# Kernel optimization log

Hardware: AMD Instinct MI355X
Metric: run time of the kernel (lower is better)

Reference implementation:

```python
import jax, jax.numpy as jnp
import numpy as np

N, D, H, T = 262144, 128, 256, 4  # nodes, embed_dim, hidden_dim, num node types


def setup_inputs() -> dict:
    key = jax.random.key(0)
    ks = jax.random.split(key, 5)
    h = jax.random.normal(ks[0], (N, D), dtype=jnp.float32)
    message = jax.random.normal(ks[1], (N, D), dtype=jnp.float32)
    node_type_ids = jax.random.randint(ks[2], (N,), 0, T, dtype=jnp.int32)
    # Spectrally-normalized linear weights are just fixed matrices at eval time;
    # scale so spectral norm is O(1).
    W1 = jax.random.normal(ks[3], (T, 2 * D, H), dtype=jnp.float32) / np.sqrt(2 * D)
    b1 = jnp.zeros((T, H), dtype=jnp.float32)
    W2 = jax.random.normal(ks[4], (T, H, D), dtype=jnp.float32) / np.sqrt(H)
    b2 = jnp.zeros((T, D), dtype=jnp.float32)
    return {"h": h, "message": message, "node_type_ids": node_type_ids,
            "W1": W1, "b1": b1, "W2": W2, "b2": b2}


def reference(h, message, node_type_ids, W1, b1, W2, b2):
    # x : (N, 2d) concatenated node state and message
    x = jnp.concatenate([h, message], axis=-1)
    dh = jnp.zeros_like(h)
    # Loop over the small fixed set of node types (T=4); each iteration is a
    # dense 2-layer SiLU MLP, results routed back by boolean mask (the torch
    # code's gather -> MLP -> scatter, expressed as compute-all + select).
    for t in range(T):
        y = jax.nn.silu(x @ W1[t] + b1[t]) @ W2[t] + b2[t]  # (N, d)
        mask = (node_type_ids == t)[:, None]
        dh = jnp.where(mask, y, dh)
    return dh
```

## Files before the change

### kernel.cpp

```cpp
#include <hip/hip_runtime.h>
#include <hip/hip_bf16.h>
#include <stdint.h>

#define N_NODES 262144
#define DDIM 128
#define KDIM 256
#define HDIM 256
#define NTYPE 4
#define BM 64
#define NB 1024

typedef float  f32x4  __attribute__((ext_vector_type(4)));
typedef short  bf16x8 __attribute__((ext_vector_type(8)));
typedef unsigned short u16x4 __attribute__((ext_vector_type(4)));


__device__ __forceinline__ unsigned short f2b(float v) {
    unsigned int u = __builtin_bit_cast(unsigned int, v);
    u += 0x7FFFu + ((u >> 16) & 1u);
    return (unsigned short)(u >> 16);
}

__global__ void k_prep(const float* __restrict__ W1, const float* __restrict__ W2,
                       unsigned short* __restrict__ W1T, unsigned short* __restrict__ W2T) {
    int tid = blockIdx.x * blockDim.x + threadIdx.x;
    const int n1 = NTYPE * HDIM * KDIM;
    for (int i = tid; i < n1; i += gridDim.x * blockDim.x) {
        int t = i / (HDIM * KDIM);
        int rem = i % (HDIM * KDIM);
        int hh = rem / KDIM;
        int k  = rem % KDIM;
        W1T[i] = f2b(W1[((size_t)t * KDIM + k) * HDIM + hh]);
    }
    const int n2 = NTYPE * DDIM * HDIM;
    for (int i = tid; i < n2; i += gridDim.x * blockDim.x) {
        int t = i / (DDIM * HDIM);
        int rem = i % (DDIM * HDIM);
        int d = rem / HDIM;
        int k = rem % HDIM;
        W2T[i] = f2b(W2[((size_t)t * HDIM + k) * DDIM + d]);
    }
}

__global__ void k_hist(const int* __restrict__ ids, int* __restrict__ bcnt) {
    __shared__ int cnt[NTYPE];
    int tid = threadIdx.x, lane = tid & 63;
    if (tid < NTYPE) cnt[tid] = 0;
    __syncthreads();
    int t = ids[blockIdx.x * 256 + tid];
    #pragma unroll
    for (int tt = 0; tt < NTYPE; ++tt) {
        unsigned long long m = __ballot(t == tt);
        if (lane == 0) atomicAdd(&cnt[tt], (int)__popcll(m));
    }
    __syncthreads();
    if (tid < NTYPE) bcnt[tid * NB + blockIdx.x] = cnt[tid];
}

__global__ __launch_bounds__(1024) void k_scan(const int* __restrict__ bcnt,
                                               int* __restrict__ gbase, int* __restrict__ meta) {
    __shared__ int wpart[16];
    __shared__ int ttot[NTYPE + 1];
    int tid = threadIdx.x, lane = tid & 63, wv = tid >> 6;
    if (tid == 0) ttot[0] = 0;
    for (int t = 0; t < NTYPE; ++t) {
        int v = bcnt[t * NB + tid];
        int s = v;
        #pragma unroll
        for (int d = 1; d < 64; d <<= 1) {
            int u = __shfl_up(s, d, 64);
            if (lane >= d) s += u;
        }
        if (lane == 63) wpart[wv] = s;
        __syncthreads();
        if (tid == 0) {
            int a = 0;
            for (int w = 0; w < 16; ++w) { int x = wpart[w]; wpart[w] = a; a += x; }
            ttot[t + 1] = ttot[t] + a;
        }
        __syncthreads();
        gbase[t * NB + tid] = ttot[t] + wpart[wv] + (s - v);
        __syncthreads();
    }
    if (tid == 0) {
        int off = 0, toff = 0;
        for (int t = 0; t < NTYPE; ++t) {
            int c = ttot[t + 1] - ttot[t];
            meta[4 + t] = off;
            meta[9 + t] = toff;
            off  += c;
            toff += (c + BM - 1) / BM;
        }
        meta[8]  = off;
        meta[13] = toff;
    }
}

__global__ void k_scatter(const int* __restrict__ ids, const int* __restrict__ gbase,
                          int* __restrict__ perm) {
    __shared__ int wb[4][NTYPE];
    int tid = threadIdx.x, lane = tid & 63, wv = tid >> 6;
    int i = blockIdx.x * 256 + tid;
    int t = ids[i];
    #pragma unroll
    for (int tt = 0; tt < NTYPE; ++tt) {
        unsigned long long m = __ballot(t == tt);
        if (lane == 0) wb[wv][tt] = (int)__popcll(m);
    }
    __syncthreads();
    if (tid < NTYPE) {
        int a = 0;
        for (int w = 0; w < 4; ++w) { int x = wb[w][tid]; wb[w][tid] = a; a += x; }
    }
    __syncthreads();
    #pragma unroll
    for (int tt = 0; tt < NTYPE; ++tt) {
        unsigned long long m = __ballot(t == tt);
        if (t == tt) {
            int rank = (int)__popcll(m & ((1ull << lane) - 1ull));
            perm[gbase[tt * NB + blockIdx.x] + wb[wv][tt] + rank] = i;
        }
    }
}

__global__ __launch_bounds__(256) void k_mlp(
        const float* __restrict__ hbuf, const float* __restrict__ mbuf,
        const float* __restrict__ b1,   const float* __restrict__ b2,
        const int* __restrict__ meta,   const int* __restrict__ perm,
        const unsigned short* __restrict__ W1T, const unsigned short* __restrict__ W2T,
        float* __restrict__ dh) {
    __shared__ unsigned short lds[BM * KDIM];

    int b = blockIdx.x;
    if (b >= meta[13]) return;
    int t = 0;
    #pragma unroll
    for (int tt = 1; tt < NTYPE; ++tt) t += (b >= meta[9 + tt]);
    int row0   = meta[4 + t] + (b - meta[9 + t]) * BM;
    int segend = meta[4 + t + 1];

    int tid = threadIdx.x, lane = tid & 63, w = tid >> 6;
    int lr = lane & 15, lg = lane >> 4;

    int c = lane;
    #pragma unroll
    for (int j = 0; j < 16; ++j) {
        int r = w + 4 * j;
        int p = row0 + r;
        int node = perm[p < N_NODES ? p : N_NODES - 1];
        const float* src = (c < 32) ? (hbuf + (size_t)node * DDIM + c * 4)
                                    : (mbuf + (size_t)node * DDIM + (c - 32) * 4);
        float4 v = *reinterpret_cast<const float4*>(src);
        u16x4 o;
        o.x = f2b(v.x); o.y = f2b(v.y); o.z = f2b(v.z); o.w = f2b(v.w);
        int soff = (r * KDIM + c * 4) ^ ((r & 7) << 3);
        *reinterpret_cast<u16x4*>(&lds[soff]) = o;
    }
    __syncthreads();

    f32x4 acc[4][4];
    #pragma unroll
    for (int ht = 0; ht < 4; ++ht)
        #pragma unroll
        for (int mt = 0; mt < 4; ++mt)
            acc[ht][mt] = (f32x4){0.f, 0.f, 0.f, 0.f};

    const unsigned short* W1p = W1T + (size_t)t * HDIM * KDIM + (size_t)(w * 64) * KDIM;
    #pragma unroll
    for (int kt = 0; kt < KDIM / 32; ++kt) {
        int kk = kt * 32 + lg * 8;
        bf16x8 aw[4], xb[4];
        #pragma unroll
        for (int ht = 0; ht < 4; ++ht)
            aw[ht] = *reinterpret_cast<const bf16x8*>(W1p + (size_t)(ht * 16 + lr) * KDIM + kk);
        #pragma unroll
        for (int mt = 0; mt < 4; ++mt) {
            int r = mt * 16 + lr;
            int soff = (r * KDIM + kk) ^ ((r & 7) << 3);
            xb[mt] = *reinterpret_cast<const bf16x8*>(&lds[soff]);
        }
        #pragma unroll
        for (int ht = 0; ht < 4; ++ht)
            #pragma unroll
            for (int mt = 0; mt < 4; ++mt)
                acc[ht][mt] = __builtin_amdgcn_mfma_f32_16x16x32_bf16(aw[ht], xb[mt], acc[ht][mt], 0, 0, 0);
    }
    __syncthreads();

    #pragma unroll
    for (int ht = 0; ht < 4; ++ht) {
        int hcol = w * 64 + ht * 16 + lg * 4;
        f32x4 b1v = *reinterpret_cast<const f32x4*>(&b1[t * HDIM + hcol]);
        #pragma unroll
        for (int mt = 0; mt < 4; ++mt) {
            int m = mt * 16 + lr;
            u16x4 o;
            #pragma unroll
            for (int r4 = 0; r4 < 4; ++r4) {
                float z = acc[ht][mt][r4] + b1v[r4];
                float s = z / (1.f + __expf(-z));
                o[r4] = f2b(s);
            }
            int soff = (m * KDIM + hcol) ^ ((m & 7) << 3);
            *reinterpret_cast<u16x4*>(&lds[soff]) = o;
        }
    }
    __syncthreads();

    f32x4 acc2[2][4];
    #pragma unroll
    for (int dt = 0; dt < 2; ++dt)
        #pragma unroll
        for (int mt = 0; mt < 4; ++mt)
            acc2[dt][mt] = (f32x4){0.f, 0.f, 0.f, 0.f};

    const unsigned short* W2p = W2T + (size_t)t * DDIM * HDIM + (size_t)(w * 32) * HDIM;
    #pragma unroll
    for (int kt = 0; kt < HDIM / 32; ++kt) {
        int kk = kt * 32 + lg * 8;
        bf16x8 aw[2], ab[4];
        #pragma unroll
        for (int dt = 0; dt < 2; ++dt)
            aw[dt] = *reinterpret_cast<const bf16x8*>(W2p + (size_t)(dt * 16 + lr) * HDIM + kk);
        #pragma unroll
        for (int mt = 0; mt < 4; ++mt) {
            int m = mt * 16 + lr;
            int soff = (m * KDIM + kk) ^ ((m & 7) << 3);
            ab[mt] = *reinterpret_cast<const bf16x8*>(&lds[soff]);
        }
        #pragma unroll
        for (int dt = 0; dt < 2; ++dt)
            #pragma unroll
            for (int mt = 0; mt < 4; ++mt)
                acc2[dt][mt] = __builtin_amdgcn_mfma_f32_16x16x32_bf16(aw[dt], ab[mt], acc2[dt][mt], 0, 0, 0);
    }

    int nd[4];
    #pragma unroll
    for (int mt = 0; mt < 4; ++mt) {
        int p = row0 + mt * 16 + lr;
        nd[mt] = perm[p < N_NODES ? p : N_NODES - 1];
    }
    #pragma unroll
    for (int dt = 0; dt < 2; ++dt) {
        int d0 = w * 32 + dt * 16 + lg * 4;
        f32x4 b2v = *reinterpret_cast<const f32x4*>(&b2[t * DDIM + d0]);
        #pragma unroll
        for (int mt = 0; mt < 4; ++mt) {
            int p = row0 + mt * 16 + lr;
            if (p < segend) {
                f32x4 v = acc2[dt][mt] + b2v;
                *reinterpret_cast<f32x4*>(&dh[(size_t)nd[mt] * DDIM + d0]) = v;
            }
        }
    }
}

extern "C" void kernel_launch(void* const* d_in, const int* in_sizes, int n_in,
                              void* d_out, int out_size, void* d_ws, size_t ws_size,
                              hipStream_t stream) {
    const float* h   = (const float*)d_in[0];
    const float* msg = (const float*)d_in[1];
    const int*   ids = (const int*)d_in[2];
    const float* W1  = (const float*)d_in[3];
    const float* b1  = (const float*)d_in[4];
    const float* W2  = (const float*)d_in[5];
    const float* b2  = (const float*)d_in[6];
    float* dh = (float*)d_out;

    char* ws = (char*)d_ws;
    int* meta  = (int*)ws;
    int* perm  = (int*)(ws + 128);
    int* bcnt  = (int*)(ws + 128 + (size_t)N_NODES * 4);
    int* gbase = bcnt + NTYPE * NB;
    unsigned short* W1T = (unsigned short*)(gbase + NTYPE * NB);
    unsigned short* W2T = W1T + (size_t)NTYPE * HDIM * KDIM;

    k_prep<<<512, 256, 0, stream>>>(W1, W2, W1T, W2T);
    k_hist<<<NB, 256, 0, stream>>>(ids, bcnt);
    k_scan<<<1, 1024, 0, stream>>>(bcnt, gbase, meta);
    k_scatter<<<NB, 256, 0, stream>>>(ids, gbase, perm);
    k_mlp<<<N_NODES / BM + NTYPE, 256, 0, stream>>>(h, msg, b1, b2, meta, perm, W1T, W2T, dh);
}
```

Baseline: 451.9 us.

## Fuse prep and histogram kernels, split LDS buffers, batch weight loads in MLP

Merges the weight-transpose kernel and the type histogram into one launch, with extra blocks handling the weight conversion, which saves one launch. In the MLP kernel, the activation tile gets its own LDS buffer instead of reusing the input tile buffer, so one barrier can be dropped. W1 fragments are now loaded in batches of four k-steps and all W2 fragments are preloaded before the second GEMM, aiming to overlap global loads with compute. This raises register and LDS use (64 KB per block), and launch_bounds(256,2) asks for two blocks per CU, which may force register spills.

```diff
diff --git a/kernel.cpp b/kernel.cpp
--- a/kernel.cpp
+++ b/kernel.cpp
@@ -21,40 +21,43 @@
     return (unsigned short)(u >> 16);
 }
 
-__global__ void k_prep(const float* __restrict__ W1, const float* __restrict__ W2,
-                       unsigned short* __restrict__ W1T, unsigned short* __restrict__ W2T) {
-    int tid = blockIdx.x * blockDim.x + threadIdx.x;
-    const int n1 = NTYPE * HDIM * KDIM;
-    for (int i = tid; i < n1; i += gridDim.x * blockDim.x) {
-        int t = i / (HDIM * KDIM);
-        int rem = i % (HDIM * KDIM);
-        int hh = rem / KDIM;
-        int k  = rem % KDIM;
-        W1T[i] = f2b(W1[((size_t)t * KDIM + k) * HDIM + hh]);
-    }
-    const int n2 = NTYPE * DDIM * HDIM;
-    for (int i = tid; i < n2; i += gridDim.x * blockDim.x) {
-        int t = i / (DDIM * HDIM);
-        int rem = i % (DDIM * HDIM);
-        int d = rem / HDIM;
-        int k = rem % HDIM;
-        W2T[i] = f2b(W2[((size_t)t * HDIM + k) * DDIM + d]);
-    }
-}
-
-__global__ void k_hist(const int* __restrict__ ids, int* __restrict__ bcnt) {
+__global__ void k_prep_hist(const int* __restrict__ ids,
+                            const float* __restrict__ W1, const float* __restrict__ W2,
+                            int* __restrict__ bcnt,
+                            unsigned short* __restrict__ W1T, unsigned short* __restrict__ W2T) {
     __shared__ int cnt[NTYPE];
-    int tid = threadIdx.x, lane = tid & 63;
-    if (tid < NTYPE) cnt[tid] = 0;
-    __syncthreads();
-    int t = ids[blockIdx.x * 256 + tid];
-    #pragma unroll
-    for (int tt = 0; tt < NTYPE; ++tt) {
-        unsigned long long m = __ballot(t == tt);
-        if (lane == 0) atomicAdd(&cnt[tt], (int)__popcll(m));
-    }
-    __syncthreads();
-    if (tid < NTYPE) bcnt[tid * NB + blockIdx.x] = cnt[tid];
+    if (blockIdx.x < NB) {
+        int tid = threadIdx.x, lane = tid & 63;
+        if (tid < NTYPE) cnt[tid] = 0;
+        __syncthreads();
+        int t = ids[blockIdx.x * 256 + tid];
+        #pragma unroll
+        for (int tt = 0; tt < NTYPE; ++tt) {
+            unsigned long long m = __ballot(t == tt);
+            if (lane == 0) atomicAdd(&cnt[tt], (int)__popcll(m));
+        }
+        __syncthreads();
+        if (tid < NTYPE) bcnt[tid * NB + blockIdx.x] = cnt[tid];
+    } else {
+        int tid = (blockIdx.x - NB) * 256 + threadIdx.x;
+        const int stride = 256 * 256;
+        const int n1 = NTYPE * HDIM * KDIM;
+        for (int i = tid; i < n1; i += stride) {
+            int t = i / (HDIM * KDIM);
+            int rem = i % (HDIM * KDIM);
+            int hh = rem / KDIM;
+            int k  = rem % KDIM;
+            W1T[i] = f2b(W1[((size_t)t * KDIM + k) * HDIM + hh]);
+        }
+        const int n2 = NTYPE * DDIM * HDIM;
+        for (int i = tid; i < n2; i += stride) {
+            int t = i / (DDIM * HDIM);
+            int rem = i % (DDIM * HDIM);
+            int d = rem / HDIM;
+            int k = rem % HDIM;
+            W2T[i] = f2b(W2[((size_t)t * HDIM + k) * DDIM + d]);
+        }
+    }
 }
 
 __global__ __launch_bounds__(1024) void k_scan(const int* __restrict__ bcnt,
@@ -123,13 +126,14 @@
     }
 }
 
-__global__ __launch_bounds__(256) void k_mlp(
+__global__ __launch_bounds__(256, 2) void k_mlp(
         const float* __restrict__ hbuf, const float* __restrict__ mbuf,
         const float* __restrict__ b1,   const float* __restrict__ b2,
         const int* __restrict__ meta,   const int* __restrict__ perm,
         const unsigned short* __restrict__ W1T, const unsigned short* __restrict__ W2T,
         float* __restrict__ dh) {
-    __shared__ unsigned short lds[BM * KDIM];
+    __shared__ unsigned short xls[BM * KDIM];
+    __shared__ unsigned short als[BM * HDIM];
 
     int b = blockIdx.x;
     if (b >= meta[13]) return;
@@ -154,9 +158,8 @@
         u16x4 o;
         o.x = f2b(v.x); o.y = f2b(v.y); o.z = f2b(v.z); o.w = f2b(v.w);
         int soff = (r * KDIM + c * 4) ^ ((r & 7) << 3);
-        *reinterpret_cast<u16x4*>(&lds[soff]) = o;
-    }
-    __syncthreads();
+        *reinterpret_cast<u16x4*>(&xls[soff]) = o;
+    }
 
     f32x4 acc[4][4];
     #pragma unroll
@@ -165,32 +168,40 @@
         for (int mt = 0; mt < 4; ++mt)
             acc[ht][mt] = (f32x4){0.f, 0.f, 0.f, 0.f};
 
-    const unsigned short* W1p = W1T + (size_t)t * HDIM * KDIM + (size_t)(w * 64) * KDIM;
-    #pragma unroll
-    for (int kt = 0; kt < KDIM / 32; ++kt) {
-        int kk = kt * 32 + lg * 8;
-        bf16x8 aw[4], xb[4];
+    const unsigned short* W1p = W1T + ((size_t)t * HDIM + w * 64) * KDIM;
+    __syncthreads();
+
+    #pragma unroll
+    for (int kh = 0; kh < 2; ++kh) {
+        bf16x8 aw[4][4];
         #pragma unroll
         for (int ht = 0; ht < 4; ++ht)
-            aw[ht] = *reinterpret_cast<const bf16x8*>(W1p + (size_t)(ht * 16 + lr) * KDIM + kk);
-        #pragma unroll
-        for (int mt = 0; mt < 4; ++mt) {
-            int r = mt * 16 + lr;
-            int soff = (r * KDIM + kk) ^ ((r & 7) << 3);
-            xb[mt] = *reinterpret_cast<const bf16x8*>(&lds[soff]);
-        }
-        #pragma unroll
-        for (int ht = 0; ht < 4; ++ht)
-            #pragma unroll
-            for (int mt = 0; mt < 4; ++mt)
-                acc[ht][mt] = __builtin_amdgcn_mfma_f32_16x16x32_bf16(aw[ht], xb[mt], acc[ht][mt], 0, 0, 0);
-    }
-    __syncthreads();
+            #pragma unroll
+            for (int kt = 0; kt < 4; ++kt)
+                aw[ht][kt] = *reinterpret_cast<const bf16x8*>(
+                    W1p + (size_t)(ht * 16 + lr) * KDIM + (kh * 4 + kt) * 32 + lg * 8);
+        #pragma unroll
+        for (int kt = 0; kt < 4; ++kt) {
+            int kk = (kh * 4 + kt) * 32 + lg * 8;
+            bf16x8 xb[4];
+            #pragma unroll
+            for (int mt = 0; mt < 4; ++mt) {
+                int m = mt * 16 + lr;
+                int soff = (m * KDIM + kk) ^ ((m & 7) << 3);
+                xb[mt] = *reinterpret_cast<const bf16x8*>(&xls[soff]);
+            }
+            #pragma unroll
+            for (int ht = 0; ht < 4; ++ht)
+                #pragma unroll
+                for (int mt = 0; mt < 4; ++mt)
+                    acc[ht][mt] = __builtin_amdgcn_mfma_f32_16x16x32_bf16(aw[ht][kt], xb[mt], acc[ht][mt], 0, 0, 0);
+        }
+    }
 
     #pragma unroll
     for (int ht = 0; ht < 4; ++ht) {
-        int hcol = w * 64 + ht * 16 + lg * 4;
-        f32x4 b1v = *reinterpret_cast<const f32x4*>(&b1[t * HDIM + hcol]);
+        int h0 = w * 64 + ht * 16 + lg * 4;
+        f32x4 b1v = *reinterpret_cast<const f32x4*>(&b1[t * HDIM + h0]);
         #pragma unroll
         for (int mt = 0; mt < 4; ++mt) {
             int m = mt * 16 + lr;
@@ -201,46 +212,50 @@
                 float s = z / (1.f + __expf(-z));
                 o[r4] = f2b(s);
             }
-            int soff = (m * KDIM + hcol) ^ ((m & 7) << 3);
-            *reinterpret_cast<u16x4*>(&lds[soff]) = o;
-        }
-    }
-    __syncthreads();
-
-    f32x4 acc2[2][4];
+            int soff = (m * HDIM + h0) ^ ((m & 7) << 3);
+            *reinterpret_cast<u16x4*>(&als[soff]) = o;
+        }
+    }
+
+    const unsigned short* W2p = W2T + ((size_t)t * DDIM + w * 32) * HDIM;
+    bf16x8 aw2[2][8];
     #pragma unroll
     for (int dt = 0; dt < 2; ++dt)
         #pragma unroll
-        for (int mt = 0; mt < 4; ++mt)
-            acc2[dt][mt] = (f32x4){0.f, 0.f, 0.f, 0.f};
-
-    const unsigned short* W2p = W2T + (size_t)t * DDIM * HDIM + (size_t)(w * 32) * HDIM;
-    #pragma unroll
-    for (int kt = 0; kt < HDIM / 32; ++kt) {
-        int kk = kt * 32 + lg * 8;
-        bf16x8 aw[2], ab[4];
-        #pragma unroll
-        for (int dt = 0; dt < 2; ++dt)
-            aw[dt] = *reinterpret_cast<const bf16x8*>(W2p + (size_t)(dt * 16 + lr) * HDIM + kk);
-        #pragma unroll
-        for (int mt = 0; mt < 4; ++mt) {
-            int m = mt * 16 + lr;
-            int soff = (m * KDIM + kk) ^ ((m & 7) << 3);
-            ab[mt] = *reinterpret_cast<const bf16x8*>(&lds[soff]);
-        }
-        #pragma unroll
-        for (int dt = 0; dt < 2; ++dt)
-            #pragma unroll
-            for (int mt = 0; mt < 4; ++mt)
-                acc2[dt][mt] = __builtin_amdgcn_mfma_f32_16x16x32_bf16(aw[dt], ab[mt], acc2[dt][mt], 0, 0, 0);
-    }
-
+        for (int kt = 0; kt < 8; ++kt)
+            aw2[dt][kt] = *reinterpret_cast<const bf16x8*>(
+                W2p + (size_t)(dt * 16 + lr) * HDIM + kt * 32 + lg * 8);
     int nd[4];
     #pragma unroll
     for (int mt = 0; mt < 4; ++mt) {
         int p = row0 + mt * 16 + lr;
         nd[mt] = perm[p < N_NODES ? p : N_NODES - 1];
     }
+    __syncthreads();
+
+    f32x4 acc2[2][4];
+    #pragma unroll
+    for (int dt = 0; dt < 2; ++dt)
+        #pragma unroll
+        for (int mt = 0; mt < 4; ++mt)
+            acc2[dt][mt] = (f32x4){0.f, 0.f, 0.f, 0.f};
+    #pragma unroll
+    for (int kt = 0; kt < 8; ++kt) {
+        int kk = kt * 32 + lg * 8;
+        bf16x8 ab[4];
+        #pragma unroll
+        for (int mt = 0; mt < 4; ++mt) {
+            int m = mt * 16 + lr;
+            int soff = (m * HDIM + kk) ^ ((m & 7) << 3);
+            ab[mt] = *reinterpret_cast<const bf16x8*>(&als[soff]);
+        }
+        #pragma unroll
+        for (int dt = 0; dt < 2; ++dt)
+            #pragma unroll
+            for (int mt = 0; mt < 4; ++mt)
+                acc2[dt][mt] = __builtin_amdgcn_mfma_f32_16x16x32_bf16(aw2[dt][kt], ab[mt], acc2[dt][mt], 0, 0, 0);
+    }
+
     #pragma unroll
     for (int dt = 0; dt < 2; ++dt) {
         int d0 = w * 32 + dt * 16 + lg * 4;
@@ -276,8 +291,7 @@
     unsigned short* W1T = (unsigned short*)(gbase + NTYPE * NB);
     unsigned short* W2T = W1T + (size_t)NTYPE * HDIM * KDIM;
 
-    k_prep<<<512, 256, 0, stream>>>(W1, W2, W1T, W2T);
-    k_hist<<<NB, 256, 0, stream>>>(ids, bcnt);
+    k_prep_hist<<<NB + 256, 256, 0, stream>>>(ids, W1, W2, bcnt, W1T, W2T);
     k_scan<<<1, 1024, 0, stream>>>(bcnt, gbase, meta);
     k_scatter<<<NB, 256, 0, stream>>>(ids, gbase, perm);
     k_mlp<<<N_NODES / BM + NTYPE, 256, 0, stream>>>(h, msg, b1, b2, meta, perm, W1T, W2T, dh);
```

Result: no change. 446.4 us (-1.2%).
